# Optimization experiments

Hardware: AMD Instinct MI355X
Metric: run time of the kernel (lower is better)

## Reference

```python
import jax, jax.numpy as jnp
import numpy as np

D_MODEL, D_STATE, D_CONV, EXPAND = 1024, 16, 4, 2
D_INNER = EXPAND * D_MODEL
BATCH, SEQ = 2, 2048


def setup_inputs() -> dict:
    key = jax.random.key(0)
    ks = jax.random.split(key, 10)
    s = lambda fan_in: 1.0 / np.sqrt(fan_in)
    return {
        "x": jax.random.normal(ks[0], (BATCH, SEQ, D_MODEL), jnp.float32),
        "W_in": jax.random.normal(ks[1], (2 * D_INNER, D_MODEL), jnp.float32) * s(D_MODEL),
        "w_conv": jax.random.normal(ks[2], (D_INNER, D_CONV), jnp.float32) * s(D_CONV),
        "b_conv": jax.random.normal(ks[3], (D_INNER,), jnp.float32) * 0.02,
        "W_x": jax.random.normal(ks[4], (D_INNER + 2 * D_STATE, D_INNER), jnp.float32) * s(D_INNER),
        "W_dt": jax.random.normal(ks[5], (D_INNER, D_INNER), jnp.float32) * s(D_INNER),
        "b_dt": jax.random.normal(ks[6], (D_INNER,), jnp.float32) * 0.02,
        "A_log": jnp.log(jax.random.uniform(ks[7], (D_INNER, D_STATE), jnp.float32, 1e-4, 1.0)),
        "D": jnp.ones((D_INNER,), jnp.float32),
        "W_out": jax.random.normal(ks[8], (D_MODEL, D_INNER), jnp.float32) * s(D_INNER),
    }


def _depthwise_causal_conv(x, w, b):
    # x: (B, L, C), w: (C, K), causal (left-pad K-1), matches conv1d(padding=K-1)[..., :L]
    K = w.shape[1]
    L = x.shape[1]
    xp = jnp.pad(x, ((0, 0), (K - 1, 0), (0, 0)))
    out = b
    for k in range(K):  # K is tiny (4)
        out = out + xp[:, k:k + L, :] * w[:, k]
    return out


def _selective_scan(x, delta, Bm, Cm, A, Dv):
    # x, delta: (B, L, d_inner); Bm, Cm: (B, L, d_state)
    def step(state, inp):
        x_t, d_t, B_t, C_t = inp  # (B,d_inner),(B,d_inner),(B,d_state),(B,d_state)
        decay = jnp.exp(d_t[..., None] * A)          # (B, d_inner, d_state)
        state = decay * state + B_t[:, None, :] * x_t[..., None]
        y_t = jnp.einsum('bds,bs->bd', state, C_t) + x_t * Dv
        return state, y_t

    init = jnp.zeros((x.shape[0], x.shape[2], A.shape[1]), x.dtype)
    xs = tuple(jnp.swapaxes(a, 0, 1) for a in (x, delta, Bm, Cm))
    _, ys = jax.lax.scan(step, init, xs)             # ys: (L, B, d_inner)
    return jnp.swapaxes(ys, 0, 1)


def reference(x, W_in, w_conv, b_conv, W_x, W_dt, b_dt, A_log, D, W_out):
    silu = jax.nn.silu
    xz = x @ W_in.T                                   # (B, L, 2*d_inner)
    x_inner, z = jnp.split(xz, 2, axis=-1)
    x_conv = silu(_depthwise_causal_conv(x_inner, w_conv, b_conv))
    x_dbl = x_conv @ W_x.T                            # (B, L, d_inner + 2*d_state)
    delta, Bm, Cm = jnp.split(x_dbl, [D_INNER, D_INNER + D_STATE], axis=-1)
    delta = jax.nn.softplus(delta @ W_dt.T + b_dt)
    A = -jnp.exp(A_log.astype(jnp.float32))
    y = _selective_scan(x_conv, delta, Bm, Cm, A, D)
    y = y * silu(z)
    return y @ W_out.T
```

## Files before the change

kernel.cpp:

```cpp
#include <hip/hip_runtime.h>
#include <hip/hip_bf16.h>


#define BATCH 2
#define SEQ   2048
#define DM    1024
#define DI    2048
#define DS    16
#define T_TOK (BATCH * SEQ)

#define CL 64
#define NC 32

typedef __bf16 v8bf __attribute__((ext_vector_type(8)));
typedef float  v4f  __attribute__((ext_vector_type(4)));

__device__ __forceinline__ void gld16(const void* g, void* l) {
    __builtin_amdgcn_global_load_lds(
        (const __attribute__((address_space(1))) void*)g,
        (__attribute__((address_space(3))) void*)l, 16, 0, 0);
}

__device__ __forceinline__ float b2f(__hip_bfloat16 v) { return __bfloat162float(v); }

__global__ void detect_dtype(const unsigned* __restrict__ Dptr, int* __restrict__ flag) {
    if (threadIdx.x == 0 && blockIdx.x == 0)
        *flag = (Dptr[0] == 0x3F803F80u) ? 1 : 0;
}

__device__ __forceinline__ float load_in(const void* p, size_t i, int isbf) {
    return isbf ? b2f(((const __hip_bfloat16*)p)[i]) : ((const float*)p)[i];
}

#define NBIG0 (T_TOK * DM)
#define NBIG1 (4096 * DM)
#define NBIG2 (DI * DI)
#define NBIG3 (DM * DI)
__global__ void convert_big(const void* __restrict__ s0, const void* __restrict__ s1,
                            const void* __restrict__ s2, const void* __restrict__ s3,
                            __hip_bfloat16* __restrict__ d0, __hip_bfloat16* __restrict__ d1,
                            __hip_bfloat16* __restrict__ d2, __hip_bfloat16* __restrict__ d3,
                            const int* __restrict__ flag) {
    if (*flag) return;
    size_t e = ((size_t)blockIdx.x * 256 + threadIdx.x) * 8;
    const float* src; __hip_bfloat16* dst;
    if (e < NBIG0)                      { src = (const float*)s0 + e;                 dst = d0 + e; }
    else if (e < NBIG0 + NBIG1)         { e -= NBIG0; src = (const float*)s1 + e;     dst = d1 + e; }
    else if (e < NBIG0 + NBIG1 + NBIG2) { e -= NBIG0 + NBIG1; src = (const float*)s2 + e; dst = d2 + e; }
    else                                { e -= NBIG0 + NBIG1 + NBIG2; src = (const float*)s3 + e; dst = d3 + e; }
    const float4 a = *(const float4*)src;
    const float4 b = *(const float4*)(src + 4);
    __bf16 o[8] = {(__bf16)a.x,(__bf16)a.y,(__bf16)a.z,(__bf16)a.w,
                   (__bf16)b.x,(__bf16)b.y,(__bf16)b.z,(__bf16)b.w};
    *(uint4*)dst = *(uint4*)&o[0];
}

__global__ void convert_small(const void* __restrict__ wconv, const void* __restrict__ bconv,
                              const void* __restrict__ bdt, const void* __restrict__ dv,
                              __hip_bfloat16* __restrict__ wconvb, __hip_bfloat16* __restrict__ bconvb,
                              __hip_bfloat16* __restrict__ bdtb, __hip_bfloat16* __restrict__ db,
                              const int* __restrict__ flag) {
    const int isbf = *flag;
    const int i = blockIdx.x * 256 + threadIdx.x;
    if (i < 8192)        wconvb[i]        = __float2bfloat16(load_in(wconv, i, isbf));
    else if (i < 10240)  bconvb[i - 8192] = __float2bfloat16(load_in(bconv, i - 8192, isbf));
    else if (i < 12288)  bdtb[i - 10240]  = __float2bfloat16(load_in(bdt, i - 10240, isbf));
    else if (i < 14336)  db[i - 12288]    = __float2bfloat16(load_in(dv, i - 12288, isbf));
}

template <int MODE, int TN>
__global__ __launch_bounds__(256) void gemm_bt(
    const __hip_bfloat16* __restrict__ Ac, const void* __restrict__ Araw,
    const __hip_bfloat16* __restrict__ Bc, const void* __restrict__ Braw,
    void* __restrict__ out0, void* __restrict__ out1,
    const __hip_bfloat16* __restrict__ bias,
    const int* __restrict__ flag,
    int M, int N, int K)
{
    constexpr int NF = TN / 32;
    constexpr int ASLOT = 512;
    constexpr int BSLOT = TN * 4;
    __shared__ v8bf Asv[2 * ASLOT];
    __shared__ v8bf Bsv[2 * BSLOT];

    const int isbf = *flag;
    const __hip_bfloat16* A  = (isbf && Araw) ? (const __hip_bfloat16*)Araw : Ac;
    const __hip_bfloat16* Bw = (isbf && Braw) ? (const __hip_bfloat16*)Braw : Bc;

    const int nx = gridDim.x;
    const int nblk = nx * gridDim.y;
    const int id = blockIdx.y * nx + blockIdx.x;
    const int sid = (id & 7) * (nblk >> 3) + (id >> 3);
    const int bxs = sid % nx;
    const int bys = sid / nx;

    const int tid  = threadIdx.x;
    const int bm   = bys * 128;
    const int bn   = bxs * TN;
    const int w    = tid >> 6;
    const int lane = tid & 63;
    const int wm   = (w >> 1) * 64;
    const int wn   = (w & 1) * (TN / 2);
    const int lrow  = lane & 15;
    const int lquad = lane >> 4;

    v4f acc[4][NF];
#pragma unroll
    for (int i = 0; i < 4; i++)
#pragma unroll
        for (int j = 0; j < NF; j++) acc[i][j] = (v4f){0.f, 0.f, 0.f, 0.f};

    const int r0 = tid >> 2;
    const int q0 = (tid & 3) ^ ((r0 >> 1) & 3);
    const __hip_bfloat16* gA0 = A  + (size_t)(bm + r0) * K + q0 * 8;
    const __hip_bfloat16* gA1 = A  + (size_t)(bm + 64 + r0) * K + q0 * 8;
    const __hip_bfloat16* gB0 = Bw + (size_t)(bn + r0) * K + q0 * 8;
    const __hip_bfloat16* gB1 = Bw + (size_t)(bn + 64 + r0) * K + q0 * 8;
    char* lA0 = (char*)Asv + tid * 16;
    char* lA1 = (char*)Asv + 4096 + tid * 16;
    char* lB0 = (char*)Bsv + tid * 16;
    char* lB1 = (char*)Bsv + 4096 + tid * 16;

    const int swz = lquad ^ ((lrow >> 1) & 3);
    int sA[4], sB[NF];
#pragma unroll
    for (int i = 0; i < 4; i++) sA[i] = (wm + i * 16 + lrow) * 4 + swz;
#pragma unroll
    for (int i = 0; i < NF; i++) sB[i] = (wn + i * 16 + lrow) * 4 + swz;

    const int NIT = K >> 5;
    gld16(gA0, lA0);
    gld16(gA1, lA1);
    gld16(gB0, lB0);
    if (TN == 128) gld16(gB1, lB1);

    int k = 32;
    for (int it = 0; it < NIT; ++it) {
        const int cb = it & 1;
        __syncthreads();
        if (it + 1 < NIT) {
            const int pa = (cb ^ 1) * 8192;
            const int pb = (cb ^ 1) * (BSLOT * 16);
            gld16(gA0 + k, lA0 + pa);
            gld16(gA1 + k, lA1 + pa);
            gld16(gB0 + k, lB0 + pb);
            if (TN == 128) gld16(gB1 + k, lB1 + pb);
            k += 32;
        }
        const int ca = cb * ASLOT;
        const int cbb = cb * BSLOT;
        v8bf af[4], bfr[NF];
#pragma unroll
        for (int i = 0; i < 4; i++)
            af[i] = Asv[ca + sA[i]];
#pragma unroll
        for (int i = 0; i < NF; i++)
            bfr[i] = Bsv[cbb + sB[i]];
#pragma unroll
        for (int mi = 0; mi < 4; mi++)
#pragma unroll
            for (int ni = 0; ni < NF; ni++)
                acc[mi][ni] = __builtin_amdgcn_mfma_f32_16x16x32_bf16(
                    af[mi], bfr[ni], acc[mi][ni], 0, 0, 0);
    }

#pragma unroll
    for (int mi = 0; mi < 4; mi++) {
#pragma unroll
        for (int ni = 0; ni < NF; ni++) {
#pragma unroll
            for (int r = 0; r < 4; r++) {
                const int grow = bm + wm + mi * 16 + lquad * 4 + r;
                const int gcol = bn + wn + ni * 16 + lrow;
                const float v = acc[mi][ni][r];
                if (MODE == 0) {
                    ((__hip_bfloat16*)out0)[(size_t)grow * N + gcol] = __float2bfloat16(v);
                } else if (MODE == 1) {
                    if (gcol < 2048) {
                        ((__hip_bfloat16*)out0)[(size_t)grow * 2048 + gcol] = __float2bfloat16(v);
                    } else if (gcol < 2080) {
                        ((float*)out1)[(size_t)grow * 32 + (gcol - 2048)] = v;
                    }
                } else if (MODE == 2) {
                    const float x = v + b2f(bias[gcol]);
                    const float sp = (x > 15.f) ? x : __logf(1.f + __expf(x));
                    ((__hip_bfloat16*)out0)[(size_t)grow * 2048 + gcol] = __float2bfloat16(sp);
                } else {
                    if (isbf)
                        ((__hip_bfloat16*)out0)[(size_t)grow * N + gcol] = __float2bfloat16(v);
                    else
                        ((float*)out0)[(size_t)grow * N + gcol] = v;
                }
            }
        }
    }
}

__global__ void prep_A(const void* __restrict__ A_log, float* __restrict__ Amat,
                       const int* __restrict__ flag) {
    const int isbf = *flag;
    const int i = blockIdx.x * 256 + threadIdx.x;
    if (i < DI * DS) Amat[i] = -__expf(load_in(A_log, i, isbf));
}

__global__ void pad_Wx(const void* __restrict__ Wx, __hip_bfloat16* __restrict__ Wxp,
                       const int* __restrict__ flag) {
    const int isbf = *flag;
    const size_t e = ((size_t)blockIdx.x * 256 + threadIdx.x) * 8;
    if (e >= (size_t)2176 * 2048) return;
    if (e >= (size_t)2080 * 2048) {
        __bf16 z[8] = {};
        *(uint4*)(Wxp + e) = *(uint4*)&z[0];
        return;
    }
    if (isbf) {
        *(uint4*)(Wxp + e) = *(const uint4*)((const __hip_bfloat16*)Wx + e);
    } else {
        const float* src = (const float*)Wx + e;
        const float4 a = *(const float4*)src;
        const float4 b = *(const float4*)(src + 4);
        __bf16 o[8] = {(__bf16)a.x,(__bf16)a.y,(__bf16)a.z,(__bf16)a.w,
                       (__bf16)b.x,(__bf16)b.y,(__bf16)b.z,(__bf16)b.w};
        *(uint4*)(Wxp + e) = *(uint4*)&o[0];
    }
}

__global__ __launch_bounds__(256) void conv_silu(
    const __hip_bfloat16* __restrict__ xz,
    const __hip_bfloat16* __restrict__ wconv,
    const __hip_bfloat16* __restrict__ bconv,
    __hip_bfloat16* __restrict__ xconv)
{
    const int idx = blockIdx.x * 256 + threadIdx.x;
    const int c8 = (idx & 255) << 3;
    const int tg = idx >> 8;
    const int tl = tg & (SEQ - 1);

    __bf16 wl[32], bl[8];
    *(uint4*)&wl[0]  = *(const uint4*)(wconv + c8 * 4);
    *(uint4*)&wl[8]  = *(const uint4*)(wconv + c8 * 4 + 8);
    *(uint4*)&wl[16] = *(const uint4*)(wconv + c8 * 4 + 16);
    *(uint4*)&wl[24] = *(const uint4*)(wconv + c8 * 4 + 24);
    *(uint4*)&bl[0]  = *(const uint4*)(bconv + c8);

    float acc[8];
#pragma unroll
    for (int cc = 0; cc < 8; cc++) acc[cc] = (float)bl[cc];

#pragma unroll
    for (int k = 0; k < 4; k++) {
        const int ts = tl - 3 + k;
        if (ts >= 0) {
            __bf16 xl[8];
            *(uint4*)&xl[0] = *(const uint4*)(xz + (size_t)(tg - 3 + k) * 4096 + c8);
#pragma unroll
            for (int cc = 0; cc < 8; cc++)
                acc[cc] += (float)wl[cc * 4 + k] * (float)xl[cc];
        }
    }

    __bf16 o[8];
#pragma unroll
    for (int cc = 0; cc < 8; cc++) {
        const float s = acc[cc] / (1.f + __expf(-acc[cc]));
        o[cc] = (__bf16)s;
    }
    *(uint4*)(xconv + (size_t)tg * DI + c8) = *(uint4*)&o[0];
}

__global__ __launch_bounds__(256) void scan_p1(
    const __hip_bfloat16* __restrict__ delta, const __hip_bfloat16* __restrict__ xconv,
    const float* __restrict__ BC, const float* __restrict__ Amat,
    float* __restrict__ Pws, float* __restrict__ Sws)
{
    const int d = blockIdx.x * 256 + threadIdx.x;
    const int c = blockIdx.y;
    const int b = blockIdx.z;
    const int tg0 = b * SEQ + c * CL;

    __shared__ float bc[CL * 32];
    for (int i = threadIdx.x; i < CL * 32; i += 256) bc[i] = BC[(size_t)tg0 * 32 + i];
    __syncthreads();

    float Areg[DS];
#pragma unroll
    for (int s = 0; s < DS; s++) Areg[s] = Amat[d * DS + s];

    float P[DS], S[DS];
#pragma unroll
    for (int s = 0; s < DS; s++) { P[s] = 1.f; S[s] = 0.f; }

    for (int i = 0; i < CL; i++) {
        const size_t tg = tg0 + i;
        const float dl = b2f(delta[tg * DI + d]);
        const float x  = b2f(xconv[tg * DI + d]);
#pragma unroll
        for (int s = 0; s < DS; s++) {
            const float e = __expf(dl * Areg[s]);
            P[s] *= e;
            S[s] = e * S[s] + bc[i * 32 + s] * x;
        }
    }

    const size_t base = (((size_t)b * NC + c) * DI + d) * DS;
#pragma unroll
    for (int s = 0; s < DS; s += 4) {
        *(float4*)(Pws + base + s) = make_float4(P[s], P[s+1], P[s+2], P[s+3]);
        *(float4*)(Sws + base + s) = make_float4(S[s], S[s+1], S[s+2], S[s+3]);
    }
}

__global__ void scan_p2(float* __restrict__ Pws, float* __restrict__ Sws) {
    const int idx = blockIdx.x * 256 + threadIdx.x;
    const int b  = idx >> 15;
    const int ds = idx & 32767;
    float carry = 0.f;
    for (int c = 0; c < NC; c++) {
        const size_t a = (((size_t)b * NC + c) << 15) + ds;
        const float p  = Pws[a];
        const float sv = Sws[a];
        Sws[a] = carry;
        carry = p * carry + sv;
    }
}

__global__ __launch_bounds__(256) void scan_p3(
    const __hip_bfloat16* __restrict__ delta, const __hip_bfloat16* __restrict__ xconv,
    const float* __restrict__ BC, const float* __restrict__ Amat,
    const float* __restrict__ Sws, const __hip_bfloat16* __restrict__ xz,
    const __hip_bfloat16* __restrict__ Dv, __hip_bfloat16* __restrict__ yg)
{
    const int d = blockIdx.x * 256 + threadIdx.x;
    const int c = blockIdx.y;
    const int b = blockIdx.z;
    const int tg0 = b * SEQ + c * CL;

    __shared__ float bc[CL * 32];
    for (int i = threadIdx.x; i < CL * 32; i += 256) bc[i] = BC[(size_t)tg0 * 32 + i];
    __syncthreads();

    float Areg[DS];
#pragma unroll
    for (int s = 0; s < DS; s++) Areg[s] = Amat[d * DS + s];

    const size_t base = (((size_t)b * NC + c) * DI + d) * DS;
    float S[DS];
#pragma unroll
    for (int s = 0; s < DS; s += 4) {
        const float4 v = *(const float4*)(Sws + base + s);
        S[s] = v.x; S[s+1] = v.y; S[s+2] = v.z; S[s+3] = v.w;
    }
    const float Dd = b2f(Dv[d]);

    for (int i = 0; i < CL; i++) {
        const size_t tg = tg0 + i;
        const float dl = b2f(delta[tg * DI + d]);
        const float x  = b2f(xconv[tg * DI + d]);
        float y = 0.f;
#pragma unroll
        for (int s = 0; s < DS; s++) {
            const float e = __expf(dl * Areg[s]);
            S[s] = e * S[s] + bc[i * 32 + s] * x;
            y += S[s] * bc[i * 32 + 16 + s];
        }
        y += x * Dd;
        const float z = b2f(xz[tg * 4096 + 2048 + d]);
        const float g = z / (1.f + __expf(-z));
        yg[tg * DI + d] = __float2bfloat16(y * g);
    }
}

extern "C" void kernel_launch(void* const* d_in, const int* in_sizes, int n_in,
                              void* d_out, int out_size, void* d_ws, size_t ws_size,
                              hipStream_t stream)
{
    const void* x_raw     = d_in[0];
    const void* W_in_raw  = d_in[1];
    const void* wconv_raw = d_in[2];
    const void* bconv_raw = d_in[3];
    const void* W_x_raw   = d_in[4];
    const void* W_dt_raw  = d_in[5];
    const void* b_dt_raw  = d_in[6];
    const void* A_log_raw = d_in[7];
    const void* D_raw     = d_in[8];
    const void* W_out_raw = d_in[9];

    char* ws = (char*)d_ws;
    size_t off = 0;
    auto alloc = [&](size_t bytes) { char* p = ws + off; off += (bytes + 255) & ~(size_t)255; return p; };
    int*            FLAG  = (int*)alloc(256);
    __hip_bfloat16* XB    = (__hip_bfloat16*)alloc((size_t)T_TOK * DM * 2);
    __hip_bfloat16* WINB  = (__hip_bfloat16*)alloc((size_t)4096 * DM * 2);
    __hip_bfloat16* WDTB  = (__hip_bfloat16*)alloc((size_t)DI * DI * 2);
    __hip_bfloat16* WOUTB = (__hip_bfloat16*)alloc((size_t)DM * DI * 2);
    __hip_bfloat16* WCONVB= (__hip_bfloat16*)alloc((size_t)DI * 4 * 2);
    __hip_bfloat16* BCONVB= (__hip_bfloat16*)alloc((size_t)DI * 2);
    __hip_bfloat16* BDTB  = (__hip_bfloat16*)alloc((size_t)DI * 2);
    __hip_bfloat16* DB    = (__hip_bfloat16*)alloc((size_t)DI * 2);
    __hip_bfloat16* XZ    = (__hip_bfloat16*)alloc((size_t)T_TOK * 4096 * 2);
    __hip_bfloat16* XCONV = (__hip_bfloat16*)alloc((size_t)T_TOK * DI * 2);
    __hip_bfloat16* DRAW  = (__hip_bfloat16*)alloc((size_t)T_TOK * DI * 2);
    __hip_bfloat16* WXPAD = (__hip_bfloat16*)alloc((size_t)2176 * DI * 2);
    float*          BC    = (float*)alloc((size_t)T_TOK * 32 * 4);
    __hip_bfloat16* DELTA = (__hip_bfloat16*)alloc((size_t)T_TOK * DI * 2);
    float*          AMAT  = (float*)alloc((size_t)DI * DS * 4);
    float*          PWS   = (float*)alloc((size_t)BATCH * NC * DI * DS * 4);
    float*          SWS   = (float*)alloc((size_t)BATCH * NC * DI * DS * 4);
    __hip_bfloat16* YG    = (__hip_bfloat16*)alloc((size_t)T_TOK * DI * 2);

    detect_dtype<<<1, 64, 0, stream>>>((const unsigned*)D_raw, FLAG);
    convert_big<<<(NBIG0 + NBIG1 + NBIG2 + NBIG3) / (256 * 8), 256, 0, stream>>>(
        x_raw, W_in_raw, W_dt_raw, W_out_raw, XB, WINB, WDTB, WOUTB, FLAG);
    convert_small<<<56, 256, 0, stream>>>(wconv_raw, bconv_raw, b_dt_raw, D_raw,
                                          WCONVB, BCONVB, BDTB, DB, FLAG);
    prep_A<<<(DI * DS + 255) / 256, 256, 0, stream>>>(A_log_raw, AMAT, FLAG);
    pad_Wx<<<(int)(((size_t)2176 * 2048 / 8 + 255) / 256), 256, 0, stream>>>(W_x_raw, WXPAD, FLAG);

    gemm_bt<0, 128><<<dim3(32, 32), 256, 0, stream>>>(
        XB, x_raw, WINB, W_in_raw, XZ, nullptr, nullptr, FLAG, T_TOK, 4096, DM);

    conv_silu<<<T_TOK, 256, 0, stream>>>(XZ, WCONVB, BCONVB, XCONV);

    gemm_bt<1, 128><<<dim3(17, 32), 256, 0, stream>>>(
        XCONV, nullptr, WXPAD, nullptr, DRAW, BC, nullptr, FLAG, T_TOK, 2176, DI);

    gemm_bt<2, 128><<<dim3(16, 32), 256, 0, stream>>>(
        DRAW, nullptr, WDTB, W_dt_raw, DELTA, nullptr, BDTB, FLAG, T_TOK, DI, DI);

    scan_p1<<<dim3(DI / 256, NC, BATCH), 256, 0, stream>>>(DELTA, XCONV, BC, AMAT, PWS, SWS);
    scan_p2<<<(BATCH * DI * DS) / 256, 256, 0, stream>>>(PWS, SWS);
    scan_p3<<<dim3(DI / 256, NC, BATCH), 256, 0, stream>>>(DELTA, XCONV, BC, AMAT, SWS, XZ, DB, YG);

    gemm_bt<3, 64><<<dim3(16, 32), 256, 0, stream>>>(
        YG, nullptr, WOUTB, W_out_raw, d_out, nullptr, nullptr, FLAG, T_TOK, DM, DI);
}
```

Before: 465.4 us.

## Use 64-row GEMM tiles and split-K for output projection to fill more CUs

```diff
diff --git a/kernel.cpp b/kernel.cpp
--- a/kernel.cpp
+++ b/kernel.cpp
@@ -68,17 +68,18 @@
     else if (i < 14336)  db[i - 12288]    = __float2bfloat16(load_in(dv, i - 12288, isbf));
 }
 
-template <int MODE, int TN>
+template <int MODE, int TM, int TN>
 __global__ __launch_bounds__(256) void gemm_bt(
     const __hip_bfloat16* __restrict__ Ac, const void* __restrict__ Araw,
     const __hip_bfloat16* __restrict__ Bc, const void* __restrict__ Braw,
     void* __restrict__ out0, void* __restrict__ out1,
     const __hip_bfloat16* __restrict__ bias,
     const int* __restrict__ flag,
-    int M, int N, int K)
+    int M, int N, int K, int LDK)
 {
+    constexpr int MF = TM / 32;
     constexpr int NF = TN / 32;
-    constexpr int ASLOT = 512;
+    constexpr int ASLOT = TM * 4;
     constexpr int BSLOT = TN * 4;
     __shared__ v8bf Asv[2 * ASLOT];
     __shared__ v8bf Bsv[2 * BSLOT];
@@ -95,42 +96,44 @@
     const int bys = sid / nx;
 
     const int tid  = threadIdx.x;
-    const int bm   = bys * 128;
+    const int bm   = bys * TM;
     const int bn   = bxs * TN;
     const int w    = tid >> 6;
     const int lane = tid & 63;
-    const int wm   = (w >> 1) * 64;
+    const int wm   = (w >> 1) * (TM / 2);
     const int wn   = (w & 1) * (TN / 2);
     const int lrow  = lane & 15;
     const int lquad = lane >> 4;
 
-    v4f acc[4][NF];
-#pragma unroll
-    for (int i = 0; i < 4; i++)
+    const int koff = (MODE == 4) ? blockIdx.z * K : 0;
+
+    v4f acc[MF][NF];
+#pragma unroll
+    for (int i = 0; i < MF; i++)
 #pragma unroll
         for (int j = 0; j < NF; j++) acc[i][j] = (v4f){0.f, 0.f, 0.f, 0.f};
 
     const int r0 = tid >> 2;
     const int q0 = (tid & 3) ^ ((r0 >> 1) & 3);
-    const __hip_bfloat16* gA0 = A  + (size_t)(bm + r0) * K + q0 * 8;
-    const __hip_bfloat16* gA1 = A  + (size_t)(bm + 64 + r0) * K + q0 * 8;
-    const __hip_bfloat16* gB0 = Bw + (size_t)(bn + r0) * K + q0 * 8;
-    const __hip_bfloat16* gB1 = Bw + (size_t)(bn + 64 + r0) * K + q0 * 8;
+    const __hip_bfloat16* gA0 = A  + (size_t)(bm + r0) * LDK + koff + q0 * 8;
+    const __hip_bfloat16* gA1 = A  + (size_t)(bm + 64 + r0) * LDK + koff + q0 * 8;
+    const __hip_bfloat16* gB0 = Bw + (size_t)(bn + r0) * LDK + koff + q0 * 8;
+    const __hip_bfloat16* gB1 = Bw + (size_t)(bn + 64 + r0) * LDK + koff + q0 * 8;
     char* lA0 = (char*)Asv + tid * 16;
     char* lA1 = (char*)Asv + 4096 + tid * 16;
     char* lB0 = (char*)Bsv + tid * 16;
     char* lB1 = (char*)Bsv + 4096 + tid * 16;
 
     const int swz = lquad ^ ((lrow >> 1) & 3);
-    int sA[4], sB[NF];
-#pragma unroll
-    for (int i = 0; i < 4; i++) sA[i] = (wm + i * 16 + lrow) * 4 + swz;
+    int sA[MF], sB[NF];
+#pragma unroll
+    for (int i = 0; i < MF; i++) sA[i] = (wm + i * 16 + lrow) * 4 + swz;
 #pragma unroll
     for (int i = 0; i < NF; i++) sB[i] = (wn + i * 16 + lrow) * 4 + swz;
 
     const int NIT = K >> 5;
     gld16(gA0, lA0);
-    gld16(gA1, lA1);
+    if (TM == 128) gld16(gA1, lA1);
     gld16(gB0, lB0);
     if (TN == 128) gld16(gB1, lB1);
 
@@ -139,25 +142,25 @@
         const int cb = it & 1;
         __syncthreads();
         if (it + 1 < NIT) {
-            const int pa = (cb ^ 1) * 8192;
+            const int pa = (cb ^ 1) * (ASLOT * 16);
             const int pb = (cb ^ 1) * (BSLOT * 16);
             gld16(gA0 + k, lA0 + pa);
-            gld16(gA1 + k, lA1 + pa);
+            if (TM == 128) gld16(gA1 + k, lA1 + pa);
             gld16(gB0 + k, lB0 + pb);
             if (TN == 128) gld16(gB1 + k, lB1 + pb);
             k += 32;
         }
         const int ca = cb * ASLOT;
         const int cbb = cb * BSLOT;
-        v8bf af[4], bfr[NF];
-#pragma unroll
-        for (int i = 0; i < 4; i++)
+        v8bf af[MF], bfr[NF];
+#pragma unroll
+        for (int i = 0; i < MF; i++)
             af[i] = Asv[ca + sA[i]];
 #pragma unroll
         for (int i = 0; i < NF; i++)
             bfr[i] = Bsv[cbb + sB[i]];
 #pragma unroll
-        for (int mi = 0; mi < 4; mi++)
+        for (int mi = 0; mi < MF; mi++)
 #pragma unroll
             for (int ni = 0; ni < NF; ni++)
                 acc[mi][ni] = __builtin_amdgcn_mfma_f32_16x16x32_bf16(
@@ -165,7 +168,7 @@
     }
 
 #pragma unroll
-    for (int mi = 0; mi < 4; mi++) {
+    for (int mi = 0; mi < MF; mi++) {
 #pragma unroll
         for (int ni = 0; ni < NF; ni++) {
 #pragma unroll
@@ -185,14 +188,31 @@
                     const float x = v + b2f(bias[gcol]);
                     const float sp = (x > 15.f) ? x : __logf(1.f + __expf(x));
                     ((__hip_bfloat16*)out0)[(size_t)grow * 2048 + gcol] = __float2bfloat16(sp);
-                } else {
+                } else if (MODE == 3) {
                     if (isbf)
                         ((__hip_bfloat16*)out0)[(size_t)grow * N + gcol] = __float2bfloat16(v);
                     else
                         ((float*)out0)[(size_t)grow * N + gcol] = v;
+                } else {
+                    ((float*)out0)[(size_t)blockIdx.z * M * N + (size_t)grow * N + gcol] = v;
                 }
             }
         }
+    }
+}
+
+__global__ void reduce_g4(const float* __restrict__ p, void* __restrict__ out,
+                          const int* __restrict__ flag, int n) {
+    const int i = (blockIdx.x * 256 + threadIdx.x) * 4;
+    if (i >= n) return;
+    const float4 a = *(const float4*)(p + i);
+    const float4 b = *(const float4*)(p + n + i);
+    const float s0 = a.x + b.x, s1 = a.y + b.y, s2 = a.z + b.z, s3 = a.w + b.w;
+    if (*flag) {
+        __bf16 o[4] = {(__bf16)s0, (__bf16)s1, (__bf16)s2, (__bf16)s3};
+        *(uint2*)((__hip_bfloat16*)out + i) = *(uint2*)&o[0];
+    } else {
+        *(float4*)((float*)out + i) = make_float4(s0, s1, s2, s3);
     }
 }
 
@@ -416,21 +436,23 @@
     prep_A<<<(DI * DS + 255) / 256, 256, 0, stream>>>(A_log_raw, AMAT, FLAG);
     pad_Wx<<<(int)(((size_t)2176 * 2048 / 8 + 255) / 256), 256, 0, stream>>>(W_x_raw, WXPAD, FLAG);
 
-    gemm_bt<0, 128><<<dim3(32, 32), 256, 0, stream>>>(
-        XB, x_raw, WINB, W_in_raw, XZ, nullptr, nullptr, FLAG, T_TOK, 4096, DM);
+    gemm_bt<0, 128, 128><<<dim3(32, 32), 256, 0, stream>>>(
+        XB, x_raw, WINB, W_in_raw, XZ, nullptr, nullptr, FLAG, T_TOK, 4096, DM, DM);
 
     conv_silu<<<T_TOK, 256, 0, stream>>>(XZ, WCONVB, BCONVB, XCONV);
 
-    gemm_bt<1, 128><<<dim3(17, 32), 256, 0, stream>>>(
-        XCONV, nullptr, WXPAD, nullptr, DRAW, BC, nullptr, FLAG, T_TOK, 2176, DI);
-
-    gemm_bt<2, 128><<<dim3(16, 32), 256, 0, stream>>>(
-        DRAW, nullptr, WDTB, W_dt_raw, DELTA, nullptr, BDTB, FLAG, T_TOK, DI, DI);
+    gemm_bt<1, 64, 128><<<dim3(17, 64), 256, 0, stream>>>(
+        XCONV, nullptr, WXPAD, nullptr, DRAW, BC, nullptr, FLAG, T_TOK, 2176, DI, DI);
+
+    gemm_bt<2, 64, 128><<<dim3(16, 64), 256, 0, stream>>>(
+        DRAW, nullptr, WDTB, W_dt_raw, DELTA, nullptr, BDTB, FLAG, T_TOK, DI, DI, DI);
 
     scan_p1<<<dim3(DI / 256, NC, BATCH), 256, 0, stream>>>(DELTA, XCONV, BC, AMAT, PWS, SWS);
     scan_p2<<<(BATCH * DI * DS) / 256, 256, 0, stream>>>(PWS, SWS);
     scan_p3<<<dim3(DI / 256, NC, BATCH), 256, 0, stream>>>(DELTA, XCONV, BC, AMAT, SWS, XZ, DB, YG);
 
-    gemm_bt<3, 64><<<dim3(16, 32), 256, 0, stream>>>(
-        YG, nullptr, WOUTB, W_out_raw, d_out, nullptr, nullptr, FLAG, T_TOK, DM, DI);
-}
+    float* G4P = (float*)XZ;
+    gemm_bt<4, 64, 128><<<dim3(8, 64, 2), 256, 0, stream>>>(
+        YG, nullptr, WOUTB, W_out_raw, G4P, nullptr, nullptr, FLAG, T_TOK, DM, DI / 2, DI);
+    reduce_g4<<<(T_TOK * DM / 4 + 255) / 256, 256, 0, stream>>>(G4P, d_out, FLAG, T_TOK * DM);
+}
```

Measured after the change: 481.8 us. 3.5% more time.
